# Performance work log

Measured on AMD Instinct MI355X. Metric: run time of the kernel, lower is better.

## Reference

```python
import jax, jax.numpy as jnp
import numpy as np

B = 16        # number of point clouds
N_PER = 2048  # points per cloud
K = 16        # knn neighbors
NUM_CLASSES = 40


def setup_inputs() -> dict:
    key = jax.random.key(0)
    ks = jax.random.split(key, 12)
    N = B * N_PER
    pos = jax.random.normal(ks[0], (N, 3), jnp.float32)
    normal = jax.random.normal(ks[1], (N, 3), jnp.float32)
    normal = normal / jnp.linalg.norm(normal, axis=1, keepdims=True)
    batch = jnp.arange(N, dtype=jnp.int32) // N_PER
    s = 0.1
    return {
        "pos": pos, "normal": normal, "batch": batch,
        # conv1 local_nn: Linear(4,32) -> ReLU -> Linear(32,32)
        "W1a": jax.random.normal(ks[2], (4, 32), jnp.float32) * s,
        "b1a": jnp.zeros((32,), jnp.float32),
        "W1b": jax.random.normal(ks[3], (32, 32), jnp.float32) * s,
        "b1b": jnp.zeros((32,), jnp.float32),
        # conv2 local_nn: Linear(36,32) -> ReLU -> Linear(32,32)
        "W2a": jax.random.normal(ks[4], (36, 32), jnp.float32) * s,
        "b2a": jnp.zeros((32,), jnp.float32),
        "W2b": jax.random.normal(ks[5], (32, 32), jnp.float32) * s,
        "b2b": jnp.zeros((32,), jnp.float32),
        # classifier: Linear(32, 40)
        "Wc": jax.random.normal(ks[6], (32, NUM_CLASSES), jnp.float32) * s,
        "bc": jnp.zeros((NUM_CLASSES,), jnp.float32),
    }


def _angle(v1, v2):
    cross = jnp.cross(v1, v2)
    return jnp.arctan2(jnp.linalg.norm(cross, axis=-1), jnp.sum(v1 * v2, axis=-1))


def _ppf(pos_i, pos_j, n_i, n_j):
    d = pos_j - pos_i
    return jnp.stack([
        jnp.linalg.norm(d, axis=-1),
        _angle(n_i, d),
        _angle(n_j, d),
        _angle(n_i, n_j),
    ], axis=-1)


def _mlp(x, Wa, ba, Wb, bb):
    return jax.nn.relu(x @ Wa + ba) @ Wb + bb


def reference(pos, normal, batch, W1a, b1a, W1b, b1b, W2a, b2a, W2b, b2b, Wc, bc):
    N = pos.shape[0]
    # --- knn_graph(k=16, loop=False) per cloud (equal-size clouds) ---
    p = pos.reshape(B, N_PER, 3)
    d2 = jnp.sum((p[:, :, None, :] - p[:, None, :, :]) ** 2, axis=-1)  # [B,n,n]
    d2 = jnp.where(jnp.eye(N_PER, dtype=bool), jnp.inf, d2)            # no self loop
    _, nbr = jax.lax.top_k(-d2, K)                                      # [B,n,K]
    nbr_g = (nbr + (jnp.arange(B) * N_PER)[:, None, None]).reshape(N, K)

    pos_j = pos[nbr_g]      # [N,K,3]
    n_j = normal[nbr_g]     # [N,K,3]
    ppf = _ppf(pos[:, None, :], pos_j, normal[:, None, :], n_j)  # [N,K,4]

    # conv1: message = PPF only (Linear(4,32)), max aggregation, relu
    h = jax.nn.relu(jnp.max(_mlp(ppf, W1a, b1a, W1b, b1b), axis=1))  # [N,32]
    # conv2: message = [h_j, ppf] (Linear(36,32)), max aggregation, relu
    msg2 = jnp.concatenate([h[nbr_g], ppf], axis=-1)                  # [N,K,36]
    h2 = jax.nn.relu(jnp.max(_mlp(msg2, W2a, b2a, W2b, b2b), axis=1))  # [N,32]

    # global max pool per cloud + classifier
    pooled = jnp.max(h2.reshape(B, N_PER, 32), axis=1)  # [B,32]
    return pooled @ Wc + bc
```

## Files before the change

kernel.cpp:

```cpp
#include <hip/hip_runtime.h>
#include <math.h>


#define NPER 2048
#define NCLOUD 16

#define OFF_NBR  (size_t)(0u)
#define OFF_PPF  (size_t)(2u << 20)
#define OFF_H    (size_t)(10u << 20)
#define OFF_G    (size_t)(14u << 20)
#define OFF_H2   (size_t)(18u << 20)
#define OFF_POOL (size_t)(22u << 20)

__device__ __forceinline__ float med3(float a, float b, float c) {
    return __builtin_amdgcn_fmed3f(a, b, c);
}
__device__ __forceinline__ void cex(float& a, float& b) {
    const float lo = fminf(a, b), hi = fmaxf(a, b); a = lo; b = hi;
}
__device__ __forceinline__ void bmerge16(float (&v)[16]) {
#pragma unroll
    for (int i = 0; i < 8; ++i) cex(v[i], v[i + 8]);
#pragma unroll
    for (int b = 0; b < 16; b += 8)
#pragma unroll
        for (int i = 0; i < 4; ++i) cex(v[b + i], v[b + i + 4]);
#pragma unroll
    for (int b = 0; b < 16; b += 4)
#pragma unroll
        for (int i = 0; i < 2; ++i) cex(v[b + i], v[b + i + 2]);
#pragma unroll
    for (int b = 0; b < 16; b += 2) cex(v[b], v[b + 1]);
}

__device__ __forceinline__ float angf(float ax, float ay, float az,
                                      float bx, float by, float bz) {
    const float cx = ay * bz - az * by;
    const float cy = az * bx - ax * bz;
    const float cz = ax * by - ay * bx;
    const float cn = sqrtf(cx * cx + cy * cy + cz * cz);
    const float dt = ax * bx + ay * by + az * bz;
    return atan2f(cn, dt);
}

__global__ __launch_bounds__(256) void knn_ppf(const float* __restrict__ pos,
                                               const float* __restrict__ nrm,
                                               int* __restrict__ nbr,
                                               float* __restrict__ ppf) {
    const int tid = threadIdx.x;
    const int pl  = tid >> 3;
    const int sl  = tid & 7;
    const int gp  = blockIdx.x * 32 + pl;
    const int cloud = gp >> 11;
    const int lp  = gp & 2047;
    const int cbase = cloud * NPER;

    __shared__ float4 tile[2048];
    __shared__ int    hiL[32][40];
    __shared__ int    cnt[32];

    if (tid < 32) cnt[tid] = 0;

#pragma unroll
    for (int c = 0; c < 8; ++c) {
        const int idx = c * 256 + tid;
        const float x = pos[(cbase + idx) * 3 + 0];
        const float y = pos[(cbase + idx) * 3 + 1];
        const float z = pos[(cbase + idx) * 3 + 2];
        tile[idx] = make_float4(x, y, z, x * x + y * y + z * z);
    }
    __syncthreads();

    const float4 P  = tile[lp];
    const float pn2 = P.w;
    const float m2x = -2.f * P.x, m2y = -2.f * P.y, m2z = -2.f * P.z;

    float dl[8];
#pragma unroll
    for (int m = 0; m < 8; ++m) dl[m] = INFINITY;

#pragma unroll 4
    for (int jj = 0; jj < 256; ++jj) {
        const int cand = jj * 8 + sl;
        const float4 C = tile[cand];
        float s = fmaf(m2x, C.x, fmaf(m2y, C.y, fmaf(m2z, C.z, C.w)));
        s = (cand == lp) ? INFINITY : s;
#pragma unroll
        for (int m = 7; m >= 1; --m) dl[m] = med3(dl[m - 1], dl[m], s);
        dl[0] = fminf(dl[0], s);
    }

    float v[16];
#pragma unroll
    for (int i = 0; i < 8; ++i) v[i] = dl[i];
#pragma unroll
    for (int i = 0; i < 8; ++i) v[15 - i] = __shfl_xor(dl[i], 1);
    bmerge16(v);
    {
        float p[16];
#pragma unroll
        for (int i = 0; i < 16; ++i) p[i] = __shfl_xor(v[i], 2);
        float w[16];
#pragma unroll
        for (int i = 0; i < 16; ++i) w[i] = fminf(v[i], p[15 - i]);
        bmerge16(w);
#pragma unroll
        for (int i = 0; i < 16; ++i) v[i] = w[i];
    }
    float tau_s;
    {
        float p[16];
#pragma unroll
        for (int i = 0; i < 16; ++i) p[i] = __shfl_xor(v[i], 4);
        float t = -INFINITY;
#pragma unroll
        for (int i = 0; i < 16; ++i) t = fmaxf(t, fminf(v[i], p[15 - i]));
        tau_s = t;
    }
    const float tsw = tau_s + 6e-5f * (1.f + pn2 + fabsf(tau_s + pn2));

#pragma unroll 4
    for (int jj = 0; jj < 256; ++jj) {
        const int cand = jj * 8 + sl;
        const float4 C = tile[cand];
        const float s = fmaf(m2x, C.x, fmaf(m2y, C.y, fmaf(m2z, C.z, C.w)));
        if (s <= tsw && cand != lp) {
            const int k = atomicAdd(&cnt[pl], 1);
            if (k < 40) hiL[pl][k] = cand;
        }
    }
    __syncthreads();

    if (tid < 32) {
        int n = cnt[tid];
        n = n > 40 ? 40 : n;
        if (n != 16) {
            const int myl = (blockIdx.x * 32 + tid) & 2047;
            const float4 Q = tile[myl];
            unsigned long long keys[16];
#pragma unroll
            for (int m = 0; m < 16; ++m) keys[m] = ~0ULL;
            for (int i = 0; i < n; ++i) {
                const int cand = hiL[tid][i];
                const float4 C = tile[cand];
                const float dx = __fsub_rn(Q.x, C.x);
                const float dy = __fsub_rn(Q.y, C.y);
                const float dz = __fsub_rn(Q.z, C.z);
                const float d2 = __fadd_rn(__fadd_rn(__fmul_rn(dx, dx),
                                                     __fmul_rn(dy, dy)),
                                           __fmul_rn(dz, dz));
                const unsigned long long key =
                    ((unsigned long long)__float_as_uint(d2) << 32) |
                    (unsigned int)cand;
                if (key < keys[15]) {
#pragma unroll
                    for (int m = 15; m >= 1; --m) {
                        const bool up   = key < keys[m - 1];
                        const bool here = key < keys[m];
                        keys[m] = up ? keys[m - 1] : (here ? key : keys[m]);
                    }
                    if (key < keys[0]) keys[0] = key;
                }
            }
#pragma unroll
            for (int m = 0; m < 16; ++m)
                hiL[tid][m] = (int)(unsigned int)(keys[m] & 0xFFFFFFFFu);
        }
    }
    __syncthreads();

    const float nix = nrm[gp * 3 + 0], niy = nrm[gp * 3 + 1], niz = nrm[gp * 3 + 2];
    const float px = P.x, py = P.y, pz = P.z;
#pragma unroll
    for (int e = 0; e < 2; ++e) {
        const int m = sl * 2 + e;
        const int j = cbase + hiL[pl][m];
        nbr[gp * 16 + m] = j;
        const float pjx = pos[j * 3 + 0], pjy = pos[j * 3 + 1], pjz = pos[j * 3 + 2];
        const float njx = nrm[j * 3 + 0], njy = nrm[j * 3 + 1], njz = nrm[j * 3 + 2];
        const float dx = pjx - px, dy = pjy - py, dz = pjz - pz;
        float4 o;
        o.x = sqrtf(dx * dx + dy * dy + dz * dz);
        o.y = angf(nix, niy, niz, dx, dy, dz);
        o.z = angf(njx, njy, njz, dx, dy, dz);
        o.w = angf(nix, niy, niz, njx, njy, njz);
        ((float4*)ppf)[(size_t)gp * 16 + m] = o;
    }
}

__global__ __launch_bounds__(256, 4) void conv1_kernel(const float* __restrict__ ppf,
                                                       const float* __restrict__ W1a,
                                                       const float* __restrict__ b1a,
                                                       const float* __restrict__ W1b,
                                                       const float* __restrict__ b1b,
                                                       float* __restrict__ h) {
    const int gid    = blockIdx.x * 256 + threadIdx.x;
    const int node   = gid >> 4;
    const int lane16 = threadIdx.x & 15;

    const float4 x = ((const float4*)ppf)[gid];

    float h1[32];
#pragma unroll
    for (int o = 0; o < 32; ++o) {
        h1[o] = fmaxf(fmaf(x.x, W1a[o],
                     fmaf(x.y, W1a[32 + o],
                     fmaf(x.z, W1a[64 + o],
                     fmaf(x.w, W1a[96 + o], b1a[o])))), 0.f);
    }

#pragma unroll 1
    for (int ob = 0; ob < 4; ++ob) {
        float acc[8];
#pragma unroll
        for (int u = 0; u < 8; ++u) acc[u] = b1b[ob * 8 + u];
#pragma unroll
        for (int hh = 0; hh < 32; ++hh) {
            const float hv = h1[hh];
#pragma unroll
            for (int u = 0; u < 8; ++u)
                acc[u] = fmaf(hv, W1b[hh * 32 + ob * 8 + u], acc[u]);
        }
#pragma unroll
        for (int u = 0; u < 8; ++u) {
            float v = acc[u];
            v = fmaxf(v, __shfl_xor(v, 1));
            v = fmaxf(v, __shfl_xor(v, 2));
            v = fmaxf(v, __shfl_xor(v, 4));
            v = fmaxf(v, __shfl_xor(v, 8));
            acc[u] = fmaxf(v, 0.f);
        }
        if (lane16 == 0) {
            float4* dst = (float4*)(h + (size_t)node * 32 + ob * 8);
            dst[0] = make_float4(acc[0], acc[1], acc[2], acc[3]);
            dst[1] = make_float4(acc[4], acc[5], acc[6], acc[7]);
        }
    }
}

__global__ __launch_bounds__(256) void gfromh(const float* __restrict__ h,
                                              const float* __restrict__ W2a,
                                              const float* __restrict__ b2a,
                                              float* __restrict__ G) {
    const int n = blockIdx.x * 256 + threadIdx.x;
    float hr[32];
    const float4* row = (const float4*)(h + (size_t)n * 32);
#pragma unroll
    for (int q = 0; q < 8; ++q) {
        const float4 v = row[q];
        hr[q * 4 + 0] = v.x; hr[q * 4 + 1] = v.y; hr[q * 4 + 2] = v.z; hr[q * 4 + 3] = v.w;
    }
    float acc[32];
#pragma unroll
    for (int o = 0; o < 32; ++o) acc[o] = b2a[o];
#pragma unroll
    for (int c = 0; c < 32; ++c) {
        const float hv = hr[c];
#pragma unroll
        for (int o = 0; o < 32; ++o) acc[o] = fmaf(hv, W2a[c * 32 + o], acc[o]);
    }
    float4* go = (float4*)(G + (size_t)n * 32);
#pragma unroll
    for (int q = 0; q < 8; ++q)
        go[q] = make_float4(acc[q * 4 + 0], acc[q * 4 + 1], acc[q * 4 + 2], acc[q * 4 + 3]);
}

__global__ __launch_bounds__(256, 4) void conv2_kernel(const float* __restrict__ ppf,
                                                       const int* __restrict__ nbr,
                                                       const float* __restrict__ G,
                                                       const float* __restrict__ W2a,
                                                       const float* __restrict__ W2b,
                                                       const float* __restrict__ b2b,
                                                       float* __restrict__ h2) {
    const int gid    = blockIdx.x * 256 + threadIdx.x;
    const int node   = gid >> 4;
    const int lane16 = threadIdx.x & 15;

    const int j = nbr[gid];

    float h1[32];
    {
        const float4* gr = (const float4*)(G + (size_t)j * 32);
#pragma unroll
        for (int q = 0; q < 8; ++q) {
            const float4 v = gr[q];
            h1[q * 4 + 0] = v.x; h1[q * 4 + 1] = v.y;
            h1[q * 4 + 2] = v.z; h1[q * 4 + 3] = v.w;
        }
    }
    const float4 x = ((const float4*)ppf)[gid];
#pragma unroll
    for (int o = 0; o < 32; ++o) {
        h1[o] = fmaxf(fmaf(x.x, W2a[32 * 32 + o],
                     fmaf(x.y, W2a[33 * 32 + o],
                     fmaf(x.z, W2a[34 * 32 + o],
                     fmaf(x.w, W2a[35 * 32 + o], h1[o])))), 0.f);
    }

#pragma unroll 1
    for (int ob = 0; ob < 4; ++ob) {
        float acc[8];
#pragma unroll
        for (int u = 0; u < 8; ++u) acc[u] = b2b[ob * 8 + u];
#pragma unroll
        for (int hh = 0; hh < 32; ++hh) {
            const float hv = h1[hh];
#pragma unroll
            for (int u = 0; u < 8; ++u)
                acc[u] = fmaf(hv, W2b[hh * 32 + ob * 8 + u], acc[u]);
        }
#pragma unroll
        for (int u = 0; u < 8; ++u) {
            float v = acc[u];
            v = fmaxf(v, __shfl_xor(v, 1));
            v = fmaxf(v, __shfl_xor(v, 2));
            v = fmaxf(v, __shfl_xor(v, 4));
            v = fmaxf(v, __shfl_xor(v, 8));
            acc[u] = fmaxf(v, 0.f);
        }
        if (lane16 == 0) {
            float4* dst = (float4*)(h2 + (size_t)node * 32 + ob * 8);
            dst[0] = make_float4(acc[0], acc[1], acc[2], acc[3]);
            dst[1] = make_float4(acc[4], acc[5], acc[6], acc[7]);
        }
    }
}

__global__ __launch_bounds__(256) void pool1(const float* __restrict__ h2,
                                             int* __restrict__ pooledi) {
    const int tid  = threadIdx.x;
    const int node = blockIdx.x * 256 + tid;
    const int cloud = node >> 11;

    float pm[32];
    const float4* row = (const float4*)(h2 + (size_t)node * 32);
#pragma unroll
    for (int q = 0; q < 8; ++q) {
        const float4 v = row[q];
        pm[q * 4 + 0] = v.x; pm[q * 4 + 1] = v.y;
        pm[q * 4 + 2] = v.z; pm[q * 4 + 3] = v.w;
    }

    __shared__ float red[256][33];
    __shared__ float red2[8][33];
#pragma unroll
    for (int o = 0; o < 32; ++o) red[tid][o] = pm[o];
    __syncthreads();
    {
        const int oc = tid & 31, ch = tid >> 5;
        float m = -INFINITY;
#pragma unroll
        for (int r = 0; r < 32; ++r) m = fmaxf(m, red[ch * 32 + r][oc]);
        red2[ch][oc] = m;
    }
    __syncthreads();
    if (tid < 32) {
        float m = red2[0][tid];
#pragma unroll
        for (int c = 1; c < 8; ++c) m = fmaxf(m, red2[c][tid]);
        atomicMax(&pooledi[cloud * 32 + tid], __float_as_int(m));
    }
}

__global__ __launch_bounds__(64) void fc_kernel(const int* __restrict__ pooledi,
                                                const float* __restrict__ Wc,
                                                const float* __restrict__ bc,
                                                float* __restrict__ out) {
    const int b = blockIdx.x;
    const int tid = threadIdx.x;
    if (tid < 40) {
        float acc = bc[tid];
#pragma unroll
        for (int o = 0; o < 32; ++o)
            acc = fmaf(__int_as_float(pooledi[b * 32 + o]), Wc[o * 40 + tid], acc);
        out[b * 40 + tid] = acc;
    }
}

extern "C" void kernel_launch(void* const* d_in, const int* in_sizes, int n_in,
                              void* d_out, int out_size, void* d_ws, size_t ws_size,
                              hipStream_t stream) {
    const float* pos = (const float*)d_in[0];
    const float* nrm = (const float*)d_in[1];
    const float* W1a = (const float*)d_in[3];
    const float* b1a = (const float*)d_in[4];
    const float* W1b = (const float*)d_in[5];
    const float* b1b = (const float*)d_in[6];
    const float* W2a = (const float*)d_in[7];
    const float* b2a = (const float*)d_in[8];
    const float* W2b = (const float*)d_in[9];
    const float* b2b = (const float*)d_in[10];
    const float* Wc  = (const float*)d_in[11];
    const float* bc  = (const float*)d_in[12];
    float* out = (float*)d_out;

    char* ws = (char*)d_ws;
    int*   nbr = (int*)(ws + OFF_NBR);
    float* ppf = (float*)(ws + OFF_PPF);
    float* h   = (float*)(ws + OFF_H);
    float* G   = (float*)(ws + OFF_G);
    float* h2  = (float*)(ws + OFF_H2);
    int*   pli = (int*)(ws + OFF_POOL);

    hipLaunchKernelGGL(knn_ppf,      dim3(1024), dim3(256), 0, stream, pos, nrm, nbr, ppf);
    hipLaunchKernelGGL(conv1_kernel, dim3(2048), dim3(256), 0, stream, ppf, W1a, b1a, W1b, b1b, h);
    hipLaunchKernelGGL(gfromh,       dim3(128),  dim3(256), 0, stream, h, W2a, b2a, G);
    hipLaunchKernelGGL(conv2_kernel, dim3(2048), dim3(256), 0, stream, ppf, nbr, G, W2a, W2b, b2b, h2);
    hipLaunchKernelGGL(pool1,        dim3(128),  dim3(256), 0, stream, h2, pli);
    hipLaunchKernelGGL(fc_kernel,    dim3(16),   dim3(64),  0, stream, pli, Wc, bc, out);
}
```

Baseline: 202.8 us.

## Fuse kNN with conv1 and G projection, and conv2 with global pooling

Merges the kNN/PPF kernel with conv1 and the h·W2a projection so that each point's 16 neighbours map onto 16 lanes. This removes the ppf reload and the round trips of the intermediate h buffer, and reads neighbour positions from the shared tile. conv2 now does the per-cloud max pooling in-block through shared memory and atomics, which drops the h2 buffer and the separate pool kernel. The kNN scan is re-split to 16 lanes per point with 4-entry lists and an extra merge stage. This doubles the number of blocks and so doubles the shared-tile loads from global memory.

```diff
diff --git a/kernel.cpp b/kernel.cpp
--- a/kernel.cpp
+++ b/kernel.cpp
@@ -7,16 +7,24 @@
 
 #define OFF_NBR  (size_t)(0u)
 #define OFF_PPF  (size_t)(2u << 20)
-#define OFF_H    (size_t)(10u << 20)
-#define OFF_G    (size_t)(14u << 20)
-#define OFF_H2   (size_t)(18u << 20)
-#define OFF_POOL (size_t)(22u << 20)
+#define OFF_G    (size_t)(10u << 20)
+#define OFF_POOL (size_t)(14u << 20)
 
 __device__ __forceinline__ float med3(float a, float b, float c) {
     return __builtin_amdgcn_fmed3f(a, b, c);
 }
 __device__ __forceinline__ void cex(float& a, float& b) {
     const float lo = fminf(a, b), hi = fmaxf(a, b); a = lo; b = hi;
+}
+__device__ __forceinline__ void bmerge8(float (&v)[8]) {
+#pragma unroll
+    for (int i = 0; i < 4; ++i) cex(v[i], v[i + 4]);
+#pragma unroll
+    for (int b = 0; b < 8; b += 4)
+#pragma unroll
+        for (int i = 0; i < 2; ++i) cex(v[b + i], v[b + i + 2]);
+#pragma unroll
+    for (int b = 0; b < 8; b += 2) cex(v[b], v[b + 1]);
 }
 __device__ __forceinline__ void bmerge16(float (&v)[16]) {
 #pragma unroll
@@ -43,23 +51,30 @@
     return atan2f(cn, dt);
 }
 
-__global__ __launch_bounds__(256) void knn_ppf(const float* __restrict__ pos,
-                                               const float* __restrict__ nrm,
-                                               int* __restrict__ nbr,
-                                               float* __restrict__ ppf) {
+__global__ __launch_bounds__(256) void knn_conv1(const float* __restrict__ pos,
+                                                 const float* __restrict__ nrm,
+                                                 const float* __restrict__ W1a,
+                                                 const float* __restrict__ b1a,
+                                                 const float* __restrict__ W1b,
+                                                 const float* __restrict__ b1b,
+                                                 const float* __restrict__ W2a,
+                                                 const float* __restrict__ b2a,
+                                                 int* __restrict__ nbr,
+                                                 float* __restrict__ ppf,
+                                                 float* __restrict__ G) {
     const int tid = threadIdx.x;
-    const int pl  = tid >> 3;
-    const int sl  = tid & 7;
-    const int gp  = blockIdx.x * 32 + pl;
+    const int pl  = tid >> 4;
+    const int sl  = tid & 15;
+    const int gp  = blockIdx.x * 16 + pl;
     const int cloud = gp >> 11;
     const int lp  = gp & 2047;
     const int cbase = cloud * NPER;
 
     __shared__ float4 tile[2048];
-    __shared__ int    hiL[32][40];
-    __shared__ int    cnt[32];
-
-    if (tid < 32) cnt[tid] = 0;
+    __shared__ int    hiL[16][40];
+    __shared__ int    cnt[16];
+
+    if (tid < 16) cnt[tid] = 0;
 
 #pragma unroll
     for (int c = 0; c < 8; ++c) {
@@ -75,53 +90,62 @@
     const float pn2 = P.w;
     const float m2x = -2.f * P.x, m2y = -2.f * P.y, m2z = -2.f * P.z;
 
-    float dl[8];
-#pragma unroll
-    for (int m = 0; m < 8; ++m) dl[m] = INFINITY;
+    float dl[4];
+#pragma unroll
+    for (int m = 0; m < 4; ++m) dl[m] = INFINITY;
 
 #pragma unroll 4
-    for (int jj = 0; jj < 256; ++jj) {
-        const int cand = jj * 8 + sl;
+    for (int jj = 0; jj < 128; ++jj) {
+        const int cand = jj * 16 + sl;
         const float4 C = tile[cand];
         float s = fmaf(m2x, C.x, fmaf(m2y, C.y, fmaf(m2z, C.z, C.w)));
         s = (cand == lp) ? INFINITY : s;
-#pragma unroll
-        for (int m = 7; m >= 1; --m) dl[m] = med3(dl[m - 1], dl[m], s);
+        dl[3] = med3(dl[2], dl[3], s);
+        dl[2] = med3(dl[1], dl[2], s);
+        dl[1] = med3(dl[0], dl[1], s);
         dl[0] = fminf(dl[0], s);
     }
 
-    float v[16];
-#pragma unroll
-    for (int i = 0; i < 8; ++i) v[i] = dl[i];
-#pragma unroll
-    for (int i = 0; i < 8; ++i) v[15 - i] = __shfl_xor(dl[i], 1);
-    bmerge16(v);
-    {
-        float p[16];
-#pragma unroll
-        for (int i = 0; i < 16; ++i) p[i] = __shfl_xor(v[i], 2);
-        float w[16];
-#pragma unroll
-        for (int i = 0; i < 16; ++i) w[i] = fminf(v[i], p[15 - i]);
-        bmerge16(w);
-#pragma unroll
-        for (int i = 0; i < 16; ++i) v[i] = w[i];
-    }
     float tau_s;
     {
-        float p[16];
-#pragma unroll
-        for (int i = 0; i < 16; ++i) p[i] = __shfl_xor(v[i], 4);
-        float t = -INFINITY;
-#pragma unroll
-        for (int i = 0; i < 16; ++i) t = fmaxf(t, fminf(v[i], p[15 - i]));
-        tau_s = t;
+        float v8[8];
+#pragma unroll
+        for (int i = 0; i < 4; ++i) v8[i] = dl[i];
+#pragma unroll
+        for (int i = 0; i < 4; ++i) v8[7 - i] = __shfl_xor(dl[i], 1);
+        bmerge8(v8);
+        float v[16];
+#pragma unroll
+        for (int i = 0; i < 8; ++i) v[i] = v8[i];
+#pragma unroll
+        for (int i = 0; i < 8; ++i) v[15 - i] = __shfl_xor(v8[i], 2);
+        bmerge16(v);
+        {
+            float p[16];
+#pragma unroll
+            for (int i = 0; i < 16; ++i) p[i] = __shfl_xor(v[i], 4);
+            float w[16];
+#pragma unroll
+            for (int i = 0; i < 16; ++i) w[i] = fminf(v[i], p[15 - i]);
+            bmerge16(w);
+#pragma unroll
+            for (int i = 0; i < 16; ++i) v[i] = w[i];
+        }
+        {
+            float p[16];
+#pragma unroll
+            for (int i = 0; i < 16; ++i) p[i] = __shfl_xor(v[i], 8);
+            float t = -INFINITY;
+#pragma unroll
+            for (int i = 0; i < 16; ++i) t = fmaxf(t, fminf(v[i], p[15 - i]));
+            tau_s = t;
+        }
     }
     const float tsw = tau_s + 6e-5f * (1.f + pn2 + fabsf(tau_s + pn2));
 
 #pragma unroll 4
-    for (int jj = 0; jj < 256; ++jj) {
-        const int cand = jj * 8 + sl;
+    for (int jj = 0; jj < 128; ++jj) {
+        const int cand = jj * 16 + sl;
         const float4 C = tile[cand];
         const float s = fmaf(m2x, C.x, fmaf(m2y, C.y, fmaf(m2z, C.z, C.w)));
         if (s <= tsw && cand != lp) {
@@ -131,11 +155,11 @@
     }
     __syncthreads();
 
-    if (tid < 32) {
+    if (tid < 16) {
         int n = cnt[tid];
         n = n > 40 ? 40 : n;
         if (n != 16) {
-            const int myl = (blockIdx.x * 32 + tid) & 2047;
+            const int myl = (blockIdx.x * 16 + tid) & 2047;
             const float4 Q = tile[myl];
             unsigned long long keys[16];
 #pragma unroll
@@ -170,35 +194,20 @@
     __syncthreads();
 
     const float nix = nrm[gp * 3 + 0], niy = nrm[gp * 3 + 1], niz = nrm[gp * 3 + 2];
-    const float px = P.x, py = P.y, pz = P.z;
-#pragma unroll
-    for (int e = 0; e < 2; ++e) {
-        const int m = sl * 2 + e;
-        const int j = cbase + hiL[pl][m];
-        nbr[gp * 16 + m] = j;
-        const float pjx = pos[j * 3 + 0], pjy = pos[j * 3 + 1], pjz = pos[j * 3 + 2];
+    float4 x;
+    {
+        const int jl = hiL[pl][sl];
+        const int j  = cbase + jl;
+        nbr[gp * 16 + sl] = j;
+        const float4 C = tile[jl];
         const float njx = nrm[j * 3 + 0], njy = nrm[j * 3 + 1], njz = nrm[j * 3 + 2];
-        const float dx = pjx - px, dy = pjy - py, dz = pjz - pz;
-        float4 o;
-        o.x = sqrtf(dx * dx + dy * dy + dz * dz);
-        o.y = angf(nix, niy, niz, dx, dy, dz);
-        o.z = angf(njx, njy, njz, dx, dy, dz);
-        o.w = angf(nix, niy, niz, njx, njy, njz);
-        ((float4*)ppf)[(size_t)gp * 16 + m] = o;
-    }
-}
-
-__global__ __launch_bounds__(256, 4) void conv1_kernel(const float* __restrict__ ppf,
-                                                       const float* __restrict__ W1a,
-                                                       const float* __restrict__ b1a,
-                                                       const float* __restrict__ W1b,
-                                                       const float* __restrict__ b1b,
-                                                       float* __restrict__ h) {
-    const int gid    = blockIdx.x * 256 + threadIdx.x;
-    const int node   = gid >> 4;
-    const int lane16 = threadIdx.x & 15;
-
-    const float4 x = ((const float4*)ppf)[gid];
+        const float dx = C.x - P.x, dy = C.y - P.y, dz = C.z - P.z;
+        x.x = sqrtf(dx * dx + dy * dy + dz * dz);
+        x.y = angf(nix, niy, niz, dx, dy, dz);
+        x.z = angf(njx, njy, njz, dx, dy, dz);
+        x.w = angf(nix, niy, niz, njx, njy, njz);
+        ((float4*)ppf)[(size_t)gp * 16 + sl] = x;
+    }
 
     float h1[32];
 #pragma unroll
@@ -209,6 +218,7 @@
                      fmaf(x.w, W1a[96 + o], b1a[o])))), 0.f);
     }
 
+    float hr[32];
 #pragma unroll 1
     for (int ob = 0; ob < 4; ++ob) {
         float acc[8];
@@ -228,53 +238,33 @@
             v = fmaxf(v, __shfl_xor(v, 2));
             v = fmaxf(v, __shfl_xor(v, 4));
             v = fmaxf(v, __shfl_xor(v, 8));
-            acc[u] = fmaxf(v, 0.f);
-        }
-        if (lane16 == 0) {
-            float4* dst = (float4*)(h + (size_t)node * 32 + ob * 8);
-            dst[0] = make_float4(acc[0], acc[1], acc[2], acc[3]);
-            dst[1] = make_float4(acc[4], acc[5], acc[6], acc[7]);
-        }
-    }
-}
-
-__global__ __launch_bounds__(256) void gfromh(const float* __restrict__ h,
-                                              const float* __restrict__ W2a,
-                                              const float* __restrict__ b2a,
-                                              float* __restrict__ G) {
-    const int n = blockIdx.x * 256 + threadIdx.x;
-    float hr[32];
-    const float4* row = (const float4*)(h + (size_t)n * 32);
-#pragma unroll
-    for (int q = 0; q < 8; ++q) {
-        const float4 v = row[q];
-        hr[q * 4 + 0] = v.x; hr[q * 4 + 1] = v.y; hr[q * 4 + 2] = v.z; hr[q * 4 + 3] = v.w;
-    }
-    float acc[32];
-#pragma unroll
-    for (int o = 0; o < 32; ++o) acc[o] = b2a[o];
-#pragma unroll
-    for (int c = 0; c < 32; ++c) {
-        const float hv = hr[c];
-#pragma unroll
-        for (int o = 0; o < 32; ++o) acc[o] = fmaf(hv, W2a[c * 32 + o], acc[o]);
-    }
-    float4* go = (float4*)(G + (size_t)n * 32);
-#pragma unroll
-    for (int q = 0; q < 8; ++q)
-        go[q] = make_float4(acc[q * 4 + 0], acc[q * 4 + 1], acc[q * 4 + 2], acc[q * 4 + 3]);
-}
-
-__global__ __launch_bounds__(256, 4) void conv2_kernel(const float* __restrict__ ppf,
-                                                       const int* __restrict__ nbr,
-                                                       const float* __restrict__ G,
-                                                       const float* __restrict__ W2a,
-                                                       const float* __restrict__ W2b,
-                                                       const float* __restrict__ b2b,
-                                                       float* __restrict__ h2) {
-    const int gid    = blockIdx.x * 256 + threadIdx.x;
-    const int node   = gid >> 4;
-    const int lane16 = threadIdx.x & 15;
+            hr[ob * 8 + u] = fmaxf(v, 0.f);
+        }
+    }
+
+    {
+        const int c0 = sl * 2;
+        float g0 = b2a[c0], g1 = b2a[c0 + 1];
+#pragma unroll
+        for (int k = 0; k < 32; ++k) {
+            g0 = fmaf(hr[k], W2a[k * 32 + c0], g0);
+            g1 = fmaf(hr[k], W2a[k * 32 + c0 + 1], g1);
+        }
+        ((float2*)(G + (size_t)gp * 32))[sl] = make_float2(g0, g1);
+    }
+}
+
+__global__ __launch_bounds__(256, 4) void conv2_pool(const float* __restrict__ ppf,
+                                                     const int* __restrict__ nbr,
+                                                     const float* __restrict__ G,
+                                                     const float* __restrict__ W2a,
+                                                     const float* __restrict__ W2b,
+                                                     const float* __restrict__ b2b,
+                                                     int* __restrict__ pooledi) {
+    const int tid    = threadIdx.x;
+    const int gid    = blockIdx.x * 256 + tid;
+    const int node16 = tid >> 4;
+    const int cloud  = blockIdx.x >> 7;
 
     const int j = nbr[gid];
 
@@ -297,6 +287,7 @@
                      fmaf(x.w, W2a[35 * 32 + o], h1[o])))), 0.f);
     }
 
+    float h2r[32];
 #pragma unroll 1
     for (int ob = 0; ob < 4; ++ob) {
         float acc[8];
@@ -316,48 +307,20 @@
             v = fmaxf(v, __shfl_xor(v, 2));
             v = fmaxf(v, __shfl_xor(v, 4));
             v = fmaxf(v, __shfl_xor(v, 8));
-            acc[u] = fmaxf(v, 0.f);
-        }
-        if (lane16 == 0) {
-            float4* dst = (float4*)(h2 + (size_t)node * 32 + ob * 8);
-            dst[0] = make_float4(acc[0], acc[1], acc[2], acc[3]);
-            dst[1] = make_float4(acc[4], acc[5], acc[6], acc[7]);
-        }
-    }
-}
-
-__global__ __launch_bounds__(256) void pool1(const float* __restrict__ h2,
-                                             int* __restrict__ pooledi) {
-    const int tid  = threadIdx.x;
-    const int node = blockIdx.x * 256 + tid;
-    const int cloud = node >> 11;
-
-    float pm[32];
-    const float4* row = (const float4*)(h2 + (size_t)node * 32);
-#pragma unroll
-    for (int q = 0; q < 8; ++q) {
-        const float4 v = row[q];
-        pm[q * 4 + 0] = v.x; pm[q * 4 + 1] = v.y;
-        pm[q * 4 + 2] = v.z; pm[q * 4 + 3] = v.w;
-    }
-
-    __shared__ float red[256][33];
-    __shared__ float red2[8][33];
-#pragma unroll
-    for (int o = 0; o < 32; ++o) red[tid][o] = pm[o];
-    __syncthreads();
-    {
-        const int oc = tid & 31, ch = tid >> 5;
-        float m = -INFINITY;
-#pragma unroll
-        for (int r = 0; r < 32; ++r) m = fmaxf(m, red[ch * 32 + r][oc]);
-        red2[ch][oc] = m;
+            h2r[ob * 8 + u] = fmaxf(v, 0.f);
+        }
+    }
+
+    __shared__ float sh[16][33];
+    if ((tid & 15) == 0) {
+#pragma unroll
+        for (int o = 0; o < 32; ++o) sh[node16][o] = h2r[o];
     }
     __syncthreads();
     if (tid < 32) {
-        float m = red2[0][tid];
-#pragma unroll
-        for (int c = 1; c < 8; ++c) m = fmaxf(m, red2[c][tid]);
+        float m = sh[0][tid];
+#pragma unroll
+        for (int n = 1; n < 16; ++n) m = fmaxf(m, sh[n][tid]);
         atomicMax(&pooledi[cloud * 32 + tid], __float_as_int(m));
     }
 }
@@ -397,15 +360,13 @@
     char* ws = (char*)d_ws;
     int*   nbr = (int*)(ws + OFF_NBR);
     float* ppf = (float*)(ws + OFF_PPF);
-    float* h   = (float*)(ws + OFF_H);
     float* G   = (float*)(ws + OFF_G);
-    float* h2  = (float*)(ws + OFF_H2);
     int*   pli = (int*)(ws + OFF_POOL);
 
-    hipLaunchKernelGGL(knn_ppf,      dim3(1024), dim3(256), 0, stream, pos, nrm, nbr, ppf);
-    hipLaunchKernelGGL(conv1_kernel, dim3(2048), dim3(256), 0, stream, ppf, W1a, b1a, W1b, b1b, h);
-    hipLaunchKernelGGL(gfromh,       dim3(128),  dim3(256), 0, stream, h, W2a, b2a, G);
-    hipLaunchKernelGGL(conv2_kernel, dim3(2048), dim3(256), 0, stream, ppf, nbr, G, W2a, W2b, b2b, h2);
-    hipLaunchKernelGGL(pool1,        dim3(128),  dim3(256), 0, stream, h2, pli);
-    hipLaunchKernelGGL(fc_kernel,    dim3(16),   dim3(64),  0, stream, pli, Wc, bc, out);
-}
+    hipLaunchKernelGGL(knn_conv1,  dim3(2048), dim3(256), 0, stream,
+                       pos, nrm, W1a, b1a, W1b, b1b, W2a, b2a, nbr, ppf, G);
+    hipLaunchKernelGGL(conv2_pool, dim3(2048), dim3(256), 0, stream,
+                       ppf, nbr, G, W2a, W2b, b2b, pli);
+    hipLaunchKernelGGL(fc_kernel,  dim3(16),   dim3(64),  0, stream,
+                       pli, Wc, bc, out);
+}
```

Result: faster. 193.6 us (-4.6%).
